# Performance work log

Hardware: AMD Instinct MI355X
Metric: run time of the kernel (lower is better)

## Reference

```python
import jax, jax.numpy as jnp
import numpy as np
from jax import lax

B = 128      # graphs per batch
N = 68       # facial landmarks (num_nodes per graph)
C = 3        # input channels
P = 32       # PATCH_SIZE
K = 16       # NUM_KERNELS
FD = 64      # feature_dim
GH = 128     # gcn_hidden_dim
OUT = 2      # output_dim
EG = 8 * N   # edges per graph
T = B * N    # total nodes


def setup_inputs() -> dict:
    key = jax.random.key(0)
    ks = jax.random.split(key, 8)
    x = jax.random.normal(ks[0], (T, C, P, P), jnp.float32)
    e = jax.random.randint(ks[1], (2, B, EG), 0, N)
    offs = (jnp.arange(B) * N)[None, :, None]
    edge_index = (e + offs).reshape(2, -1)            # within-graph edges, global ids
    batch = jnp.repeat(jnp.arange(B), N)              # node -> graph id
    conv_w = jax.random.normal(ks[2], (N, K, C, 3, 3), jnp.float32) * 0.05
    conv_b = jnp.zeros((N, K), jnp.float32)
    lin1_w = jax.random.normal(ks[3], (N, K * (P // 2) * (P // 2), FD), jnp.float32) * 0.02
    lin1_b = jnp.zeros((N, FD), jnp.float32)
    gcn_w = jax.random.normal(ks[4], (FD, GH), jnp.float32) * 0.1
    gcn_b = jnp.zeros((GH,), jnp.float32)
    mlp_w1 = jax.random.normal(ks[5], (GH, GH // 2), jnp.float32) * 0.1
    mlp_b1 = jnp.zeros((GH // 2,), jnp.float32)
    mlp_w2 = jax.random.normal(ks[6], (GH // 2, OUT), jnp.float32) * 0.1
    mlp_b2 = jnp.zeros((OUT,), jnp.float32)
    return dict(x=x, edge_index=edge_index, batch=batch, conv_w=conv_w, conv_b=conv_b,
                lin1_w=lin1_w, lin1_b=lin1_b, gcn_w=gcn_w, gcn_b=gcn_b,
                mlp_w1=mlp_w1, mlp_b1=mlp_b1, mlp_w2=mlp_w2, mlp_b2=mlp_b2)


def reference(x, edge_index, batch, conv_w, conv_b, lin1_w, lin1_b,
              gcn_w, gcn_b, mlp_w1, mlp_b1, mlp_w2, mlp_b2):
    # --- per-node-type CNN routing (nodes are laid out [graph, local_index]) ---
    xr = x.reshape(B, N, C, P, P)

    def cnn_one(xn, w, b):           # xn: [B,C,P,P]  w: [K,C,3,3]
        y = lax.conv_general_dilated(xn, w, (1, 1), 'SAME',
                                     dimension_numbers=('NCHW', 'OIHW', 'NCHW'))
        return jax.nn.relu(y + b[None, :, None, None])

    a = jax.vmap(cnn_one, in_axes=(1, 0, 0), out_axes=1)(xr, conv_w, conv_b)  # [B,N,K,P,P]
    pooled = lax.reduce_window(a, -jnp.inf, lax.max,
                               (1, 1, 1, 2, 2), (1, 1, 1, 2, 2), 'VALID')     # [B,N,K,P/2,P/2]
    flat = pooled.reshape(B, N, -1)
    feats = jax.nn.relu(jnp.einsum('bnf,nfo->bno', flat, lin1_w) + lin1_b[None])  # [B,N,FD]
    nodes = feats.reshape(T, FD)

    # --- GCNConv: add self-loops, symmetric normalization ---
    loop = jnp.arange(T)
    src = jnp.concatenate([edge_index[0], loop])
    dst = jnp.concatenate([edge_index[1], loop])
    deg = jax.ops.segment_sum(jnp.ones_like(dst, jnp.float32), dst, T)
    dis = jnp.where(deg > 0, 1.0 / jnp.sqrt(deg), 0.0)
    norm = dis[src] * dis[dst]
    xw = nodes @ gcn_w                                   # [T,GH]
    h = jax.ops.segment_sum(norm[:, None] * xw[src], dst, T) + gcn_b
    h = jax.nn.relu(h)

    # --- global mean pool over graphs ---
    cnt = jax.ops.segment_sum(jnp.ones((T,), jnp.float32), batch, B)
    g = jax.ops.segment_sum(h, batch, B) / cnt[:, None]  # [B,GH]

    # --- MLP head ---
    z = jax.nn.relu(g @ mlp_w1 + mlp_b1)
    return z @ mlp_w2 + mlp_b2                           # [B,OUT]
```

## Files before the change

kernel.cpp:

```cpp
#include <hip/hip_runtime.h>
#include <hip/hip_fp16.h>

#define B_   128
#define N_   68
#define C_   3
#define P_   32
#define K_   16
#define FD_  64
#define GH_  128
#define EG_  544
#define T_   8704
#define FLAT_ 4096
#define FCH_ 16

typedef __attribute__((ext_vector_type(8))) _Float16 half8;
typedef __attribute__((ext_vector_type(2))) _Float16 half2v;
typedef __attribute__((ext_vector_type(4))) float   floatx4;
typedef __attribute__((ext_vector_type(4))) unsigned int uint32x4;

#define ROWP 40
#define CHP  1400

__global__ __launch_bounds__(256) void wfrag_prep_kernel(
    const float* __restrict__ conv_w, _Float16* __restrict__ wfrag) {
  const int n = blockIdx.x;
  const int tid = threadIdx.x;
  const float* wp = conv_w + (size_t)n * (K_ * 27);
  _Float16* out = wfrag + (size_t)n * 2048;
  for (int i = tid; i < 2048; i += 256) {
    int sx   = (i >> 10) & 1;
    int type = (i >> 9) & 1;
    int k    = (i >> 5) & 15;
    int slot = i & 31;
    float v = 0.0f;
    if (type == 0) {
      int q = slot >> 3, r = (slot >> 2) & 1, col = slot & 3;
      int cr = q * 2 + r, c = cr / 3, dy = cr - c * 3, dx = col - sx;
      if (dx >= 0 && dx < 3) v = wp[k * 27 + c * 9 + dy * 3 + dx];
    } else {
      int q = slot >> 3, j = slot & 7;
      if (q == 0 && j < 4) {
        int dx = j - sx;
        if (dx >= 0 && dx < 3) v = wp[k * 27 + 24 + dx];
      }
    }
    out[i] = (_Float16)v;
  }
}

__global__ __launch_bounds__(256) void conv_pool_kernel(
    const float* __restrict__ x, const _Float16* __restrict__ wfrag,
    const float* __restrict__ conv_b, _Float16* __restrict__ pooled) {
  const int t = blockIdx.x;
  const int n = t % N_;
  const int tid = threadIdx.x;

  __shared__ _Float16 xsh[3 * CHP];

  const int lane = tid & 63;
  const int lr = lane & 15, q = lane >> 4;
  const int wave = tid >> 6;
  const int ldy = lr >> 3, ldx = lr & 7;

  const float4* xg = (const float4*)(x + (size_t)t * (C_ * P_ * P_));
  float4 xv[3];
  #pragma unroll
  for (int j = 0; j < 3; j++) xv[j] = xg[tid + j * 256];

  const _Float16* wf = wfrag + (size_t)n * 2048 + lr * 32 + q * 8;
  half8 aMain0 = *(const half8*)&wf[0 * 512];
  half8 aCorr0 = *(const half8*)&wf[1 * 512];
  half8 aMain1 = *(const half8*)&wf[2 * 512];
  half8 aCorr1 = *(const half8*)&wf[3 * 512];
  floatx4 cbias = *(const floatx4*)&conv_b[(size_t)n * K_ + q * 4];

  for (int i = tid; i < 396; i += 256) {
    int c = i / 132, j = i - c * 132;
    int off;
    if (j < 34)       off = j;
    else if (j < 68)  off = 33 * ROWP + (j - 34);
    else if (j < 100) off = (j - 68 + 1) * ROWP;
    else              off = (j - 100 + 1) * ROWP + 33;
    xsh[c * CHP + off] = (_Float16)0.0f;
  }
  #pragma unroll
  for (int j = 0; j < 3; j++) {
    int f0 = (tid + j * 256) * 4;
    int c = f0 >> 10, rem = f0 & 1023, y = rem >> 5, xc = rem & 31;
    _Float16* dp = &xsh[c * CHP + (y + 1) * ROWP + xc + 1];
    dp[0] = (_Float16)xv[j].x; dp[1] = (_Float16)xv[j].y;
    dp[2] = (_Float16)xv[j].z; dp[3] = (_Float16)xv[j].w;
  }
  __syncthreads();

  const int crL = q * 2, crH = crL + 1;
  const int cL = crL / 3, dyL = crL - cL * 3;
  const int cH = crH / 3, dyH = crH - cH * 3;
  const _Float16* chL = &xsh[cL * CHP + dyL * ROWP];
  const _Float16* chH = &xsh[cH * CHP + dyH * ROWP];
  const _Float16* chC = &xsh[2 * CHP + 2 * ROWP];

  #pragma unroll
  for (int i = 0; i < 4; i++) {
    const int qq = wave * 4 + i;
    const int py0 = (qq >> 1) * 2, px0 = (qq & 1) * 8;
    const int py = py0 + ldy, px = px0 + ldx;
    const int ebase = py * (2 * ROWP) + px * 2;
    const _Float16* pL = chL + ebase;
    const _Float16* pH = chH + ebase;
    const _Float16* pC = chC + ebase;

    floatx4 mx;
    #pragma unroll
    for (int sy = 0; sy < 2; sy++) {
      unsigned int uL0 = *(const unsigned int*)&pL[sy * ROWP];
      unsigned int uL1 = *(const unsigned int*)&pL[sy * ROWP + 2];
      unsigned int uH0 = *(const unsigned int*)&pH[sy * ROWP];
      unsigned int uH1 = *(const unsigned int*)&pH[sy * ROWP + 2];
      unsigned int uC0 = *(const unsigned int*)&pC[sy * ROWP];
      unsigned int uC1 = *(const unsigned int*)&pC[sy * ROWP + 2];
      half8 bMain = __builtin_bit_cast(half8, (uint32x4){uL0, uL1, uH0, uH1});
      half8 bCorr = __builtin_bit_cast(half8, (uint32x4){uC0, uC1, uC0, uC1});
      floatx4 d0 = __builtin_amdgcn_mfma_f32_16x16x32_f16(aCorr0, bCorr, cbias, 0, 0, 0);
      d0 = __builtin_amdgcn_mfma_f32_16x16x32_f16(aMain0, bMain, d0, 0, 0, 0);
      floatx4 d1 = __builtin_amdgcn_mfma_f32_16x16x32_f16(aCorr1, bCorr, cbias, 0, 0, 0);
      d1 = __builtin_amdgcn_mfma_f32_16x16x32_f16(aMain1, bMain, d1, 0, 0, 0);
      floatx4 m;
      m[0] = fmaxf(d0[0], d1[0]); m[1] = fmaxf(d0[1], d1[1]);
      m[2] = fmaxf(d0[2], d1[2]); m[3] = fmaxf(d0[3], d1[3]);
      if (sy == 0) mx = m;
      else {
        mx[0] = fmaxf(mx[0], m[0]); mx[1] = fmaxf(mx[1], m[1]);
        mx[2] = fmaxf(mx[2], m[2]); mx[3] = fmaxf(mx[3], m[3]);
      }
    }
    _Float16* op = pooled + (size_t)t * FLAT_ + q * 1024 + py * 16 + px;
    op[0]   = (_Float16)fmaxf(mx[0], 0.0f);
    op[256] = (_Float16)fmaxf(mx[1], 0.0f);
    op[512] = (_Float16)fmaxf(mx[2], 0.0f);
    op[768] = (_Float16)fmaxf(mx[3], 0.0f);
  }
}

__global__ __launch_bounds__(256) void lin1_mfma_kernel(
    const _Float16* __restrict__ pooled, const float* __restrict__ lin1_w,
    float* __restrict__ part) {
  const int n   = blockIdx.x >> 4;
  const int fc  = blockIdx.x & 15;
  const int tid = threadIdx.x;
  const int wave = tid >> 6, lane = tid & 63;
  const int q = lane >> 4, lr = lane & 15;

  __shared__ __align__(16) _Float16 As[128 * 72];
  __shared__ __align__(16) _Float16 Bt[64 * 72];

  floatx4 acc[2][4];
  #pragma unroll
  for (int mt = 0; mt < 2; mt++)
    #pragma unroll
    for (int nt = 0; nt < 4; nt++)
      acc[mt][nt] = (floatx4){0.f, 0.f, 0.f, 0.f};

  const int f_base = fc * 256;
  for (int step = 0; step < 4; step++) {
    const int f0 = f_base + step * 64;

    #pragma unroll
    for (int j = 0; j < 4; j++) {
      int idx = tid + j * 256;
      int r = idx >> 3, ch = idx & 7;
      uint4 v = *(const uint4*)&pooled[(size_t)(r * N_ + n) * FLAT_ + f0 + ch * 8];
      *(uint4*)&As[r * 72 + ch * 8] = v;
    }
    const float* wg = &lin1_w[(size_t)n * (FLAT_ * FD_) + (size_t)f0 * FD_];
    #pragma unroll
    for (int it = 0; it < 2; it++) {
      int p = tid + it * 256;
      int o0 = (p & 15) * 4, k0 = (p >> 4) * 2;
      const float* wgk = wg + k0 * 64 + o0;
      float4 va = *(const float4*)wgk;
      float4 vb = *(const float4*)(wgk + 64);
      *(half2v*)&Bt[(o0 + 0) * 72 + k0] = (half2v){(_Float16)va.x, (_Float16)vb.x};
      *(half2v*)&Bt[(o0 + 1) * 72 + k0] = (half2v){(_Float16)va.y, (_Float16)vb.y};
      *(half2v*)&Bt[(o0 + 2) * 72 + k0] = (half2v){(_Float16)va.z, (_Float16)vb.z};
      *(half2v*)&Bt[(o0 + 3) * 72 + k0] = (half2v){(_Float16)va.w, (_Float16)vb.w};
    }
    __syncthreads();

    #pragma unroll
    for (int kh = 0; kh < 2; kh++) {
      half8 af[2], bf[4];
      #pragma unroll
      for (int mt = 0; mt < 2; mt++)
        af[mt] = *(const half8*)&As[(wave * 32 + mt * 16 + lr) * 72 + kh * 32 + q * 8];
      #pragma unroll
      for (int nt = 0; nt < 4; nt++)
        bf[nt] = *(const half8*)&Bt[(nt * 16 + lr) * 72 + kh * 32 + q * 8];
      #pragma unroll
      for (int mt = 0; mt < 2; mt++)
        #pragma unroll
        for (int nt = 0; nt < 4; nt++)
          acc[mt][nt] = __builtin_amdgcn_mfma_f32_16x16x32_f16(
              af[mt], bf[nt], acc[mt][nt], 0, 0, 0);
    }
    __syncthreads();
  }

  float* pb = part + (size_t)fc * T_ * FD_;
  #pragma unroll
  for (int mt = 0; mt < 2; mt++) {
    #pragma unroll
    for (int v = 0; v < 4; v++) {
      int r = wave * 32 + mt * 16 + q * 4 + v;
      size_t base = (size_t)(r * N_ + n) * FD_;
      #pragma unroll
      for (int nt = 0; nt < 4; nt++)
        pb[base + nt * 16 + lr] = acc[mt][nt][v];
    }
  }
}

__global__ __launch_bounds__(256) void feats_kernel(
    const float* __restrict__ part, const float* __restrict__ lin1_b,
    float* __restrict__ feats) {
  int gid = blockIdx.x * 256 + threadIdx.x;
  int t = gid >> 4, f4 = (gid & 15) * 4;
  int n = t % N_;
  float4 s = *(const float4*)&lin1_b[n * FD_ + f4];
  #pragma unroll
  for (int fc = 0; fc < FCH_; fc++) {
    float4 v = *(const float4*)&part[((size_t)fc * T_ + t) * FD_ + f4];
    s.x += v.x; s.y += v.y; s.z += v.z; s.w += v.w;
  }
  s.x = fmaxf(s.x, 0.f); s.y = fmaxf(s.y, 0.f);
  s.z = fmaxf(s.z, 0.f); s.w = fmaxf(s.w, 0.f);
  *(float4*)&feats[(size_t)t * FD_ + f4] = s;
}

__global__ __launch_bounds__(256) void gcn_agg_kernel(
    const float* __restrict__ feats, const int* __restrict__ edge_index,
    float* __restrict__ agg) {
  const int b  = blockIdx.x >> 1;
  const int fh = blockIdx.x & 1;
  const int tid = threadIdx.x;

  __shared__ float fS[N_ * 33], aS[N_ * 33];
  __shared__ int   esrcS[EG_], edstS[EG_];
  __shared__ float nrmS[EG_];
  __shared__ int   degS[N_];
  __shared__ float disS[N_];

  if (tid < N_) degS[tid] = 0;
  const int* srcp = edge_index;
  const int* dstp = edge_index + (B_ * EG_);
  const int e0 = b * EG_, nbase = b * N_;
  for (int e = tid; e < EG_; e += 256) {
    esrcS[e] = srcp[e0 + e] - nbase;
    edstS[e] = dstp[e0 + e] - nbase;
  }
  for (int idx = tid; idx < N_ * 32; idx += 256) {
    int i = idx >> 5, f = idx & 31;
    fS[i * 33 + f] = feats[(size_t)(b * N_ + i) * FD_ + fh * 32 + f];
  }
  __syncthreads();
  for (int e = tid; e < EG_; e += 256) atomicAdd(&degS[edstS[e]], 1);
  __syncthreads();
  if (tid < N_) disS[tid] = rsqrtf((float)(degS[tid] + 1));
  __syncthreads();
  for (int e = tid; e < EG_; e += 256)
    nrmS[e] = disS[esrcS[e]] * disS[edstS[e]];
  for (int idx = tid; idx < N_ * 32; idx += 256) {
    int i = idx >> 5, f = idx & 31;
    float d = disS[i];
    aS[i * 33 + f] = d * d * fS[i * 33 + f];
  }
  __syncthreads();
  for (int idx = tid; idx < EG_ * 32; idx += 256) {
    int e = idx >> 5, f = idx & 31;
    atomicAdd(&aS[edstS[e] * 33 + f], nrmS[e] * fS[esrcS[e] * 33 + f]);
  }
  __syncthreads();
  for (int idx = tid; idx < N_ * 32; idx += 256) {
    int i = idx >> 5, f = idx & 31;
    agg[(size_t)(b * N_ + i) * FD_ + fh * 32 + f] = aS[i * 33 + f];
  }
}

__global__ __launch_bounds__(512) void gcn_head_kernel(
    const float* __restrict__ agg, const float* __restrict__ gcn_w,
    const float* __restrict__ gcn_b, const float* __restrict__ w1,
    const float* __restrict__ b1, const float* __restrict__ w2,
    const float* __restrict__ b2, float* __restrict__ out) {
  const int b = blockIdx.x;
  const int tid = threadIdx.x;

  __shared__ float aS[N_ * 68];
  __shared__ float wS[FD_ * GH_];
  __shared__ float gP[4][GH_];
  __shared__ float z1S[64];

  for (int i4 = tid; i4 < N_ * 16; i4 += 512) {
    int i = i4 >> 4, qf = (i4 & 15) * 4;
    *(float4*)&aS[i * 68 + qf] = *(const float4*)&agg[(size_t)(b * N_ + i) * FD_ + qf];
  }
  #pragma unroll
  for (int j = 0; j < 4; j++)
    ((float4*)wS)[tid + j * 512] = ((const float4*)gcn_w)[tid + j * 512];
  __syncthreads();

  const int j = tid & 127, ig = tid >> 7;
  float wc[64];
  #pragma unroll
  for (int k = 0; k < 64; k++) wc[k] = wS[k * GH_ + j];
  const float bias = gcn_b[j];
  float gsum = 0.f;
  for (int i = ig; i < N_; i += 4) {
    float acc = bias;
    #pragma unroll
    for (int kq = 0; kq < 16; kq++) {
      float4 a = *(const float4*)&aS[i * 68 + kq * 4];
      acc += a.x * wc[kq * 4] + a.y * wc[kq * 4 + 1]
           + a.z * wc[kq * 4 + 2] + a.w * wc[kq * 4 + 3];
    }
    gsum += fmaxf(acc, 0.f);
  }
  gP[ig][j] = gsum;
  __syncthreads();
  if (tid < GH_)
    gP[0][tid] = (gP[0][tid] + gP[1][tid] + gP[2][tid] + gP[3][tid]) * (1.f / 68.f);
  __syncthreads();
  if (tid < 64) {
    float s = b1[tid];
    #pragma unroll 8
    for (int jj = 0; jj < GH_; jj++) s += gP[0][jj] * w1[jj * 64 + tid];
    z1S[tid] = fmaxf(s, 0.f);
  }
  __syncthreads();
  if (tid < 2) {
    float s = b2[tid];
    #pragma unroll 8
    for (int jj = 0; jj < 64; jj++) s += z1S[jj] * w2[jj * 2 + tid];
    out[b * 2 + tid] = s;
  }
}

extern "C" void kernel_launch(void* const* d_in, const int* in_sizes, int n_in,
                              void* d_out, int out_size, void* d_ws, size_t ws_size,
                              hipStream_t stream) {
  const float* x        = (const float*)d_in[0];
  const int*   edge_idx = (const int*)d_in[1];
  const float* conv_w   = (const float*)d_in[3];
  const float* conv_b   = (const float*)d_in[4];
  const float* lin1_w   = (const float*)d_in[5];
  const float* lin1_b   = (const float*)d_in[6];
  const float* gcn_w    = (const float*)d_in[7];
  const float* gcn_b    = (const float*)d_in[8];
  const float* mlp_w1   = (const float*)d_in[9];
  const float* mlp_b1   = (const float*)d_in[10];
  const float* mlp_w2   = (const float*)d_in[11];
  const float* mlp_b2   = (const float*)d_in[12];
  float* outp = (float*)d_out;

  char* wsb = (char*)d_ws;
  _Float16* pooled = (_Float16*)wsb;
  float* part  = (float*)(wsb + (size_t)T_ * FLAT_ * 2);
  float* feats = part + (size_t)FCH_ * T_ * FD_;
  float* agg   = feats + (size_t)T_ * FD_;
  _Float16* wfrag = (_Float16*)(agg + (size_t)T_ * FD_);

  wfrag_prep_kernel<<<N_, 256, 0, stream>>>(conv_w, wfrag);
  conv_pool_kernel<<<T_, 256, 0, stream>>>(x, wfrag, conv_b, pooled);
  lin1_mfma_kernel<<<N_ * FCH_, 256, 0, stream>>>(pooled, lin1_w, part);
  feats_kernel<<<544, 256, 0, stream>>>(part, lin1_b, feats);
  gcn_agg_kernel<<<B_ * 2, 256, 0, stream>>>(feats, edge_idx, agg);
  gcn_head_kernel<<<B_, 512, 0, stream>>>(agg, gcn_w, gcn_b,
                                          mlp_w1, mlp_b1, mlp_w2, mlp_b2, outp);
}
```

Measured before the change: 311.8 us.

## Fuse feats, GCN aggregation and head kernels; process two nodes per conv block

Three tail kernels (partial-sum reduction, GCN aggregation, GCN head) are merged into one per-graph kernel, so the feats and agg intermediates no longer round-trip through global memory and two launches disappear. The lin1 partial outputs are re-laid out as [node][fc][feature] so the fused kernel reads one contiguous chunk per node. The conv_pool kernel now handles two nodes of the same type per block, halving the grid and reusing the weight fragment loads. The tail becomes 128 blocks doing more serial work each, and the conv kernel's shared memory per block doubles, which may lower occupancy.

```diff
diff --git a/kernel.cpp b/kernel.cpp
--- a/kernel.cpp
+++ b/kernel.cpp
@@ -10,6 +10,7 @@
 #define GH_  128
 #define EG_  544
 #define T_   8704
+#define HT_  4352
 #define FLAT_ 4096
 #define FCH_ 16
 
@@ -51,21 +52,24 @@
 __global__ __launch_bounds__(256) void conv_pool_kernel(
     const float* __restrict__ x, const _Float16* __restrict__ wfrag,
     const float* __restrict__ conv_b, _Float16* __restrict__ pooled) {
-  const int t = blockIdx.x;
-  const int n = t % N_;
+  const int t0 = blockIdx.x;
+  const int n = t0 % N_;
   const int tid = threadIdx.x;
 
-  __shared__ _Float16 xsh[3 * CHP];
+  __shared__ _Float16 xsh[2][3 * CHP];
 
   const int lane = tid & 63;
   const int lr = lane & 15, q = lane >> 4;
   const int wave = tid >> 6;
   const int ldy = lr >> 3, ldx = lr & 7;
 
-  const float4* xg = (const float4*)(x + (size_t)t * (C_ * P_ * P_));
-  float4 xv[3];
-  #pragma unroll
-  for (int j = 0; j < 3; j++) xv[j] = xg[tid + j * 256];
+  float4 xv[2][3];
+  #pragma unroll
+  for (int im = 0; im < 2; im++) {
+    const float4* xg = (const float4*)(x + (size_t)(t0 + im * HT_) * (C_ * P_ * P_));
+    #pragma unroll
+    for (int j = 0; j < 3; j++) xv[im][j] = xg[tid + j * 256];
+  }
 
   const _Float16* wf = wfrag + (size_t)n * 2048 + lr * 32 + q * 8;
   half8 aMain0 = *(const half8*)&wf[0 * 512];
@@ -74,71 +78,85 @@
   half8 aCorr1 = *(const half8*)&wf[3 * 512];
   floatx4 cbias = *(const floatx4*)&conv_b[(size_t)n * K_ + q * 4];
 
-  for (int i = tid; i < 396; i += 256) {
-    int c = i / 132, j = i - c * 132;
-    int off;
-    if (j < 34)       off = j;
-    else if (j < 68)  off = 33 * ROWP + (j - 34);
-    else if (j < 100) off = (j - 68 + 1) * ROWP;
-    else              off = (j - 100 + 1) * ROWP + 33;
-    xsh[c * CHP + off] = (_Float16)0.0f;
-  }
-  #pragma unroll
-  for (int j = 0; j < 3; j++) {
-    int f0 = (tid + j * 256) * 4;
-    int c = f0 >> 10, rem = f0 & 1023, y = rem >> 5, xc = rem & 31;
-    _Float16* dp = &xsh[c * CHP + (y + 1) * ROWP + xc + 1];
-    dp[0] = (_Float16)xv[j].x; dp[1] = (_Float16)xv[j].y;
-    dp[2] = (_Float16)xv[j].z; dp[3] = (_Float16)xv[j].w;
+  #pragma unroll
+  for (int im = 0; im < 2; im++) {
+    for (int i = tid; i < 396; i += 256) {
+      int c = i / 132, j = i - c * 132;
+      int off;
+      if (j < 34)       off = j;
+      else if (j < 68)  off = 33 * ROWP + (j - 34);
+      else if (j < 100) off = (j - 68 + 1) * ROWP;
+      else              off = (j - 100 + 1) * ROWP + 33;
+      xsh[im][c * CHP + off] = (_Float16)0.0f;
+    }
+  }
+  #pragma unroll
+  for (int im = 0; im < 2; im++) {
+    #pragma unroll
+    for (int j = 0; j < 3; j++) {
+      int f0 = (tid + j * 256) * 4;
+      int c = f0 >> 10, rem = f0 & 1023, y = rem >> 5, xc = rem & 31;
+      _Float16* dp = &xsh[im][c * CHP + (y + 1) * ROWP + xc + 1];
+      dp[0] = (_Float16)xv[im][j].x; dp[1] = (_Float16)xv[im][j].y;
+      dp[2] = (_Float16)xv[im][j].z; dp[3] = (_Float16)xv[im][j].w;
+    }
   }
   __syncthreads();
 
   const int crL = q * 2, crH = crL + 1;
   const int cL = crL / 3, dyL = crL - cL * 3;
   const int cH = crH / 3, dyH = crH - cH * 3;
-  const _Float16* chL = &xsh[cL * CHP + dyL * ROWP];
-  const _Float16* chH = &xsh[cH * CHP + dyH * ROWP];
-  const _Float16* chC = &xsh[2 * CHP + 2 * ROWP];
-
-  #pragma unroll
-  for (int i = 0; i < 4; i++) {
-    const int qq = wave * 4 + i;
-    const int py0 = (qq >> 1) * 2, px0 = (qq & 1) * 8;
-    const int py = py0 + ldy, px = px0 + ldx;
-    const int ebase = py * (2 * ROWP) + px * 2;
-    const _Float16* pL = chL + ebase;
-    const _Float16* pH = chH + ebase;
-    const _Float16* pC = chC + ebase;
-
-    floatx4 mx;
-    #pragma unroll
-    for (int sy = 0; sy < 2; sy++) {
-      unsigned int uL0 = *(const unsigned int*)&pL[sy * ROWP];
-      unsigned int uL1 = *(const unsigned int*)&pL[sy * ROWP + 2];
-      unsigned int uH0 = *(const unsigned int*)&pH[sy * ROWP];
-      unsigned int uH1 = *(const unsigned int*)&pH[sy * ROWP + 2];
-      unsigned int uC0 = *(const unsigned int*)&pC[sy * ROWP];
-      unsigned int uC1 = *(const unsigned int*)&pC[sy * ROWP + 2];
-      half8 bMain = __builtin_bit_cast(half8, (uint32x4){uL0, uL1, uH0, uH1});
-      half8 bCorr = __builtin_bit_cast(half8, (uint32x4){uC0, uC1, uC0, uC1});
-      floatx4 d0 = __builtin_amdgcn_mfma_f32_16x16x32_f16(aCorr0, bCorr, cbias, 0, 0, 0);
-      d0 = __builtin_amdgcn_mfma_f32_16x16x32_f16(aMain0, bMain, d0, 0, 0, 0);
-      floatx4 d1 = __builtin_amdgcn_mfma_f32_16x16x32_f16(aCorr1, bCorr, cbias, 0, 0, 0);
-      d1 = __builtin_amdgcn_mfma_f32_16x16x32_f16(aMain1, bMain, d1, 0, 0, 0);
-      floatx4 m;
-      m[0] = fmaxf(d0[0], d1[0]); m[1] = fmaxf(d0[1], d1[1]);
-      m[2] = fmaxf(d0[2], d1[2]); m[3] = fmaxf(d0[3], d1[3]);
-      if (sy == 0) mx = m;
-      else {
-        mx[0] = fmaxf(mx[0], m[0]); mx[1] = fmaxf(mx[1], m[1]);
-        mx[2] = fmaxf(mx[2], m[2]); mx[3] = fmaxf(mx[3], m[3]);
+  const int offL = cL * CHP + dyL * ROWP;
+  const int offH = cH * CHP + dyH * ROWP;
+  const int offC = 2 * CHP + 2 * ROWP;
+
+  #pragma unroll
+  for (int im = 0; im < 2; im++) {
+    const _Float16* chL = &xsh[im][offL];
+    const _Float16* chH = &xsh[im][offH];
+    const _Float16* chC = &xsh[im][offC];
+    const size_t tcur = (size_t)(t0 + im * HT_);
+
+    #pragma unroll
+    for (int i = 0; i < 4; i++) {
+      const int qq = wave * 4 + i;
+      const int py0 = (qq >> 1) * 2, px0 = (qq & 1) * 8;
+      const int py = py0 + ldy, px = px0 + ldx;
+      const int ebase = py * (2 * ROWP) + px * 2;
+      const _Float16* pL = chL + ebase;
+      const _Float16* pH = chH + ebase;
+      const _Float16* pC = chC + ebase;
+
+      floatx4 mx;
+      #pragma unroll
+      for (int sy = 0; sy < 2; sy++) {
+        unsigned int uL0 = *(const unsigned int*)&pL[sy * ROWP];
+        unsigned int uL1 = *(const unsigned int*)&pL[sy * ROWP + 2];
+        unsigned int uH0 = *(const unsigned int*)&pH[sy * ROWP];
+        unsigned int uH1 = *(const unsigned int*)&pH[sy * ROWP + 2];
+        unsigned int uC0 = *(const unsigned int*)&pC[sy * ROWP];
+        unsigned int uC1 = *(const unsigned int*)&pC[sy * ROWP + 2];
+        half8 bMain = __builtin_bit_cast(half8, (uint32x4){uL0, uL1, uH0, uH1});
+        half8 bCorr = __builtin_bit_cast(half8, (uint32x4){uC0, uC1, uC0, uC1});
+        floatx4 d0 = __builtin_amdgcn_mfma_f32_16x16x32_f16(aCorr0, bCorr, cbias, 0, 0, 0);
+        d0 = __builtin_amdgcn_mfma_f32_16x16x32_f16(aMain0, bMain, d0, 0, 0, 0);
+        floatx4 d1 = __builtin_amdgcn_mfma_f32_16x16x32_f16(aCorr1, bCorr, cbias, 0, 0, 0);
+        d1 = __builtin_amdgcn_mfma_f32_16x16x32_f16(aMain1, bMain, d1, 0, 0, 0);
+        floatx4 m;
+        m[0] = fmaxf(d0[0], d1[0]); m[1] = fmaxf(d0[1], d1[1]);
+        m[2] = fmaxf(d0[2], d1[2]); m[3] = fmaxf(d0[3], d1[3]);
+        if (sy == 0) mx = m;
+        else {
+          mx[0] = fmaxf(mx[0], m[0]); mx[1] = fmaxf(mx[1], m[1]);
+          mx[2] = fmaxf(mx[2], m[2]); mx[3] = fmaxf(mx[3], m[3]);
+        }
       }
-    }
-    _Float16* op = pooled + (size_t)t * FLAT_ + q * 1024 + py * 16 + px;
-    op[0]   = (_Float16)fmaxf(mx[0], 0.0f);
-    op[256] = (_Float16)fmaxf(mx[1], 0.0f);
-    op[512] = (_Float16)fmaxf(mx[2], 0.0f);
-    op[768] = (_Float16)fmaxf(mx[3], 0.0f);
+      _Float16* op = pooled + tcur * FLAT_ + q * 1024 + py * 16 + px;
+      op[0]   = (_Float16)fmaxf(mx[0], 0.0f);
+      op[256] = (_Float16)fmaxf(mx[1], 0.0f);
+      op[512] = (_Float16)fmaxf(mx[2], 0.0f);
+      op[768] = (_Float16)fmaxf(mx[3], 0.0f);
+    }
   }
 }
 
@@ -206,106 +224,73 @@
     __syncthreads();
   }
 
-  float* pb = part + (size_t)fc * T_ * FD_;
   #pragma unroll
   for (int mt = 0; mt < 2; mt++) {
     #pragma unroll
     for (int v = 0; v < 4; v++) {
       int r = wave * 32 + mt * 16 + q * 4 + v;
-      size_t base = (size_t)(r * N_ + n) * FD_;
+      size_t base = ((size_t)(r * N_ + n) * FCH_ + fc) * FD_;
       #pragma unroll
       for (int nt = 0; nt < 4; nt++)
-        pb[base + nt * 16 + lr] = acc[mt][nt][v];
-    }
-  }
-}
-
-__global__ __launch_bounds__(256) void feats_kernel(
+        part[base + nt * 16 + lr] = acc[mt][nt][v];
+    }
+  }
+}
+
+__global__ __launch_bounds__(512) void gcn_tail_kernel(
     const float* __restrict__ part, const float* __restrict__ lin1_b,
-    float* __restrict__ feats) {
-  int gid = blockIdx.x * 256 + threadIdx.x;
-  int t = gid >> 4, f4 = (gid & 15) * 4;
-  int n = t % N_;
-  float4 s = *(const float4*)&lin1_b[n * FD_ + f4];
-  #pragma unroll
-  for (int fc = 0; fc < FCH_; fc++) {
-    float4 v = *(const float4*)&part[((size_t)fc * T_ + t) * FD_ + f4];
-    s.x += v.x; s.y += v.y; s.z += v.z; s.w += v.w;
-  }
-  s.x = fmaxf(s.x, 0.f); s.y = fmaxf(s.y, 0.f);
-  s.z = fmaxf(s.z, 0.f); s.w = fmaxf(s.w, 0.f);
-  *(float4*)&feats[(size_t)t * FD_ + f4] = s;
-}
-
-__global__ __launch_bounds__(256) void gcn_agg_kernel(
-    const float* __restrict__ feats, const int* __restrict__ edge_index,
-    float* __restrict__ agg) {
-  const int b  = blockIdx.x >> 1;
-  const int fh = blockIdx.x & 1;
-  const int tid = threadIdx.x;
-
-  __shared__ float fS[N_ * 33], aS[N_ * 33];
-  __shared__ int   esrcS[EG_], edstS[EG_];
-  __shared__ float nrmS[EG_];
-  __shared__ int   degS[N_];
-  __shared__ float disS[N_];
-
-  if (tid < N_) degS[tid] = 0;
-  const int* srcp = edge_index;
-  const int* dstp = edge_index + (B_ * EG_);
-  const int e0 = b * EG_, nbase = b * N_;
-  for (int e = tid; e < EG_; e += 256) {
-    esrcS[e] = srcp[e0 + e] - nbase;
-    edstS[e] = dstp[e0 + e] - nbase;
-  }
-  for (int idx = tid; idx < N_ * 32; idx += 256) {
-    int i = idx >> 5, f = idx & 31;
-    fS[i * 33 + f] = feats[(size_t)(b * N_ + i) * FD_ + fh * 32 + f];
-  }
-  __syncthreads();
-  for (int e = tid; e < EG_; e += 256) atomicAdd(&degS[edstS[e]], 1);
-  __syncthreads();
-  if (tid < N_) disS[tid] = rsqrtf((float)(degS[tid] + 1));
-  __syncthreads();
-  for (int e = tid; e < EG_; e += 256)
-    nrmS[e] = disS[esrcS[e]] * disS[edstS[e]];
-  for (int idx = tid; idx < N_ * 32; idx += 256) {
-    int i = idx >> 5, f = idx & 31;
-    float d = disS[i];
-    aS[i * 33 + f] = d * d * fS[i * 33 + f];
-  }
-  __syncthreads();
-  for (int idx = tid; idx < EG_ * 32; idx += 256) {
-    int e = idx >> 5, f = idx & 31;
-    atomicAdd(&aS[edstS[e] * 33 + f], nrmS[e] * fS[esrcS[e] * 33 + f]);
-  }
-  __syncthreads();
-  for (int idx = tid; idx < N_ * 32; idx += 256) {
-    int i = idx >> 5, f = idx & 31;
-    agg[(size_t)(b * N_ + i) * FD_ + fh * 32 + f] = aS[i * 33 + f];
-  }
-}
-
-__global__ __launch_bounds__(512) void gcn_head_kernel(
-    const float* __restrict__ agg, const float* __restrict__ gcn_w,
+    const int* __restrict__ edge_index, const float* __restrict__ gcn_w,
     const float* __restrict__ gcn_b, const float* __restrict__ w1,
     const float* __restrict__ b1, const float* __restrict__ w2,
     const float* __restrict__ b2, float* __restrict__ out) {
   const int b = blockIdx.x;
   const int tid = threadIdx.x;
 
-  __shared__ float aS[N_ * 68];
+  __shared__ float fS[N_ * 64], aS[N_ * 64];
+  __shared__ int   esrcS[EG_], edstS[EG_];
+  __shared__ float nrmS[EG_];
+  __shared__ int   degS[N_];
+  __shared__ float disS[N_];
   __shared__ float wS[FD_ * GH_];
   __shared__ float gP[4][GH_];
   __shared__ float z1S[64];
 
-  for (int i4 = tid; i4 < N_ * 16; i4 += 512) {
-    int i = i4 >> 4, qf = (i4 & 15) * 4;
-    *(float4*)&aS[i * 68 + qf] = *(const float4*)&agg[(size_t)(b * N_ + i) * FD_ + qf];
+  if (tid < N_) degS[tid] = 0;
+  const int* srcp = edge_index;
+  const int* dstp = edge_index + (B_ * EG_);
+  const int e0 = b * EG_, nbase = b * N_;
+  for (int e = tid; e < EG_; e += 512) {
+    esrcS[e] = srcp[e0 + e] - nbase;
+    edstS[e] = dstp[e0 + e] - nbase;
   }
   #pragma unroll
   for (int j = 0; j < 4; j++)
     ((float4*)wS)[tid + j * 512] = ((const float4*)gcn_w)[tid + j * 512];
+  for (int idx = tid; idx < N_ * 64; idx += 512) {
+    int i = idx >> 6, f = idx & 63;
+    const float* pp = &part[(size_t)((b * N_ + i) * FCH_) * FD_ + f];
+    float s = lin1_b[i * FD_ + f];
+    #pragma unroll
+    for (int fc = 0; fc < FCH_; fc++) s += pp[fc * FD_];
+    fS[idx] = fmaxf(s, 0.f);
+  }
+  __syncthreads();
+  for (int e = tid; e < EG_; e += 512) atomicAdd(&degS[edstS[e]], 1);
+  __syncthreads();
+  if (tid < N_) disS[tid] = rsqrtf((float)(degS[tid] + 1));
+  __syncthreads();
+  for (int e = tid; e < EG_; e += 512)
+    nrmS[e] = disS[esrcS[e]] * disS[edstS[e]];
+  for (int idx = tid; idx < N_ * 64; idx += 512) {
+    int i = idx >> 6;
+    float d = disS[i];
+    aS[idx] = d * d * fS[idx];
+  }
+  __syncthreads();
+  for (int idx = tid; idx < EG_ * 64; idx += 512) {
+    int e = idx >> 6, f = idx & 63;
+    atomicAdd(&aS[edstS[e] * 64 + f], nrmS[e] * fS[esrcS[e] * 64 + f]);
+  }
   __syncthreads();
 
   const int j = tid & 127, ig = tid >> 7;
@@ -318,7 +303,7 @@
     float acc = bias;
     #pragma unroll
     for (int kq = 0; kq < 16; kq++) {
-      float4 a = *(const float4*)&aS[i * 68 + kq * 4];
+      float4 a = *(const float4*)&aS[i * 64 + kq * 4];
       acc += a.x * wc[kq * 4] + a.y * wc[kq * 4 + 1]
            + a.z * wc[kq * 4 + 2] + a.w * wc[kq * 4 + 3];
     }
@@ -364,15 +349,11 @@
   char* wsb = (char*)d_ws;
   _Float16* pooled = (_Float16*)wsb;
   float* part  = (float*)(wsb + (size_t)T_ * FLAT_ * 2);
-  float* feats = part + (size_t)FCH_ * T_ * FD_;
-  float* agg   = feats + (size_t)T_ * FD_;
-  _Float16* wfrag = (_Float16*)(agg + (size_t)T_ * FD_);
+  _Float16* wfrag = (_Float16*)(part + (size_t)T_ * FCH_ * FD_);
 
   wfrag_prep_kernel<<<N_, 256, 0, stream>>>(conv_w, wfrag);
-  conv_pool_kernel<<<T_, 256, 0, stream>>>(x, wfrag, conv_b, pooled);
+  conv_pool_kernel<<<HT_, 256, 0, stream>>>(x, wfrag, conv_b, pooled);
   lin1_mfma_kernel<<<N_ * FCH_, 256, 0, stream>>>(pooled, lin1_w, part);
-  feats_kernel<<<544, 256, 0, stream>>>(part, lin1_b, feats);
-  gcn_agg_kernel<<<B_ * 2, 256, 0, stream>>>(feats, edge_idx, agg);
-  gcn_head_kernel<<<B_, 512, 0, stream>>>(agg, gcn_w, gcn_b,
+  gcn_tail_kernel<<<B_, 512, 0, stream>>>(part, lin1_b, edge_idx, gcn_w, gcn_b,
                                           mlp_w1, mlp_b1, mlp_w2, mlp_b2, outp);
 }
```

New measurement: 327.9 us. 1.05x slower.

## Process two nodes per conv block and reorder lin1 partial-sum layout

Applied to the files above, without the earlier changes.

The conv+pool kernel now handles two node images per block, t0 and t0+4352. 4352 is a multiple of 68, so both share the same node type and weight fragments, and the grid is halved. This amortises the weight-fragment loads and launch overhead and raises bytes in flight per block, at the cost of twice the shared memory and more registers. Separately, the lin1 partial buffer is re-laid out as [node][chunk][feature], so the reduction in feats_kernel reads contiguous memory. In exchange, the MFMA kernel's stores become more strided.

```diff
diff --git a/kernel.cpp b/kernel.cpp
--- a/kernel.cpp
+++ b/kernel.cpp
@@ -10,6 +10,7 @@
 #define GH_  128
 #define EG_  544
 #define T_   8704
+#define HT_  4352
 #define FLAT_ 4096
 #define FCH_ 16
 
@@ -51,21 +52,24 @@
 __global__ __launch_bounds__(256) void conv_pool_kernel(
     const float* __restrict__ x, const _Float16* __restrict__ wfrag,
     const float* __restrict__ conv_b, _Float16* __restrict__ pooled) {
-  const int t = blockIdx.x;
-  const int n = t % N_;
-  const int tid = threadIdx.x;
-
-  __shared__ _Float16 xsh[3 * CHP];
+  const int t0 = blockIdx.x;
+  const int n = t0 % N_;
+  const int tid = threadIdx.x;
+
+  __shared__ _Float16 xsh[2][3 * CHP];
 
   const int lane = tid & 63;
   const int lr = lane & 15, q = lane >> 4;
   const int wave = tid >> 6;
   const int ldy = lr >> 3, ldx = lr & 7;
 
-  const float4* xg = (const float4*)(x + (size_t)t * (C_ * P_ * P_));
-  float4 xv[3];
-  #pragma unroll
-  for (int j = 0; j < 3; j++) xv[j] = xg[tid + j * 256];
+  float4 xv[2][3];
+  #pragma unroll
+  for (int im = 0; im < 2; im++) {
+    const float4* xg = (const float4*)(x + (size_t)(t0 + im * HT_) * (C_ * P_ * P_));
+    #pragma unroll
+    for (int j = 0; j < 3; j++) xv[im][j] = xg[tid + j * 256];
+  }
 
   const _Float16* wf = wfrag + (size_t)n * 2048 + lr * 32 + q * 8;
   half8 aMain0 = *(const half8*)&wf[0 * 512];
@@ -74,71 +78,85 @@
   half8 aCorr1 = *(const half8*)&wf[3 * 512];
   floatx4 cbias = *(const floatx4*)&conv_b[(size_t)n * K_ + q * 4];
 
-  for (int i = tid; i < 396; i += 256) {
-    int c = i / 132, j = i - c * 132;
-    int off;
-    if (j < 34)       off = j;
-    else if (j < 68)  off = 33 * ROWP + (j - 34);
-    else if (j < 100) off = (j - 68 + 1) * ROWP;
-    else              off = (j - 100 + 1) * ROWP + 33;
-    xsh[c * CHP + off] = (_Float16)0.0f;
-  }
-  #pragma unroll
-  for (int j = 0; j < 3; j++) {
-    int f0 = (tid + j * 256) * 4;
-    int c = f0 >> 10, rem = f0 & 1023, y = rem >> 5, xc = rem & 31;
-    _Float16* dp = &xsh[c * CHP + (y + 1) * ROWP + xc + 1];
-    dp[0] = (_Float16)xv[j].x; dp[1] = (_Float16)xv[j].y;
-    dp[2] = (_Float16)xv[j].z; dp[3] = (_Float16)xv[j].w;
+  #pragma unroll
+  for (int im = 0; im < 2; im++) {
+    for (int i = tid; i < 396; i += 256) {
+      int c = i / 132, j = i - c * 132;
+      int off;
+      if (j < 34)       off = j;
+      else if (j < 68)  off = 33 * ROWP + (j - 34);
+      else if (j < 100) off = (j - 68 + 1) * ROWP;
+      else              off = (j - 100 + 1) * ROWP + 33;
+      xsh[im][c * CHP + off] = (_Float16)0.0f;
+    }
+  }
+  #pragma unroll
+  for (int im = 0; im < 2; im++) {
+    #pragma unroll
+    for (int j = 0; j < 3; j++) {
+      int f0 = (tid + j * 256) * 4;
+      int c = f0 >> 10, rem = f0 & 1023, y = rem >> 5, xc = rem & 31;
+      _Float16* dp = &xsh[im][c * CHP + (y + 1) * ROWP + xc + 1];
+      dp[0] = (_Float16)xv[im][j].x; dp[1] = (_Float16)xv[im][j].y;
+      dp[2] = (_Float16)xv[im][j].z; dp[3] = (_Float16)xv[im][j].w;
+    }
   }
   __syncthreads();
 
   const int crL = q * 2, crH = crL + 1;
   const int cL = crL / 3, dyL = crL - cL * 3;
   const int cH = crH / 3, dyH = crH - cH * 3;
-  const _Float16* chL = &xsh[cL * CHP + dyL * ROWP];
-  const _Float16* chH = &xsh[cH * CHP + dyH * ROWP];
-  const _Float16* chC = &xsh[2 * CHP + 2 * ROWP];
-
-  #pragma unroll
-  for (int i = 0; i < 4; i++) {
-    const int qq = wave * 4 + i;
-    const int py0 = (qq >> 1) * 2, px0 = (qq & 1) * 8;
-    const int py = py0 + ldy, px = px0 + ldx;
-    const int ebase = py * (2 * ROWP) + px * 2;
-    const _Float16* pL = chL + ebase;
-    const _Float16* pH = chH + ebase;
-    const _Float16* pC = chC + ebase;
-
-    floatx4 mx;
-    #pragma unroll
-    for (int sy = 0; sy < 2; sy++) {
-      unsigned int uL0 = *(const unsigned int*)&pL[sy * ROWP];
-      unsigned int uL1 = *(const unsigned int*)&pL[sy * ROWP + 2];
-      unsigned int uH0 = *(const unsigned int*)&pH[sy * ROWP];
-      unsigned int uH1 = *(const unsigned int*)&pH[sy * ROWP + 2];
-      unsigned int uC0 = *(const unsigned int*)&pC[sy * ROWP];
-      unsigned int uC1 = *(const unsigned int*)&pC[sy * ROWP + 2];
-      half8 bMain = __builtin_bit_cast(half8, (uint32x4){uL0, uL1, uH0, uH1});
-      half8 bCorr = __builtin_bit_cast(half8, (uint32x4){uC0, uC1, uC0, uC1});
-      floatx4 d0 = __builtin_amdgcn_mfma_f32_16x16x32_f16(aCorr0, bCorr, cbias, 0, 0, 0);
-      d0 = __builtin_amdgcn_mfma_f32_16x16x32_f16(aMain0, bMain, d0, 0, 0, 0);
-      floatx4 d1 = __builtin_amdgcn_mfma_f32_16x16x32_f16(aCorr1, bCorr, cbias, 0, 0, 0);
-      d1 = __builtin_amdgcn_mfma_f32_16x16x32_f16(aMain1, bMain, d1, 0, 0, 0);
-      floatx4 m;
-      m[0] = fmaxf(d0[0], d1[0]); m[1] = fmaxf(d0[1], d1[1]);
-      m[2] = fmaxf(d0[2], d1[2]); m[3] = fmaxf(d0[3], d1[3]);
-      if (sy == 0) mx = m;
-      else {
-        mx[0] = fmaxf(mx[0], m[0]); mx[1] = fmaxf(mx[1], m[1]);
-        mx[2] = fmaxf(mx[2], m[2]); mx[3] = fmaxf(mx[3], m[3]);
+  const int offL = cL * CHP + dyL * ROWP;
+  const int offH = cH * CHP + dyH * ROWP;
+  const int offC = 2 * CHP + 2 * ROWP;
+
+  #pragma unroll
+  for (int im = 0; im < 2; im++) {
+    const _Float16* chL = &xsh[im][offL];
+    const _Float16* chH = &xsh[im][offH];
+    const _Float16* chC = &xsh[im][offC];
+    const size_t tcur = (size_t)(t0 + im * HT_);
+
+    #pragma unroll
+    for (int i = 0; i < 4; i++) {
+      const int qq = wave * 4 + i;
+      const int py0 = (qq >> 1) * 2, px0 = (qq & 1) * 8;
+      const int py = py0 + ldy, px = px0 + ldx;
+      const int ebase = py * (2 * ROWP) + px * 2;
+      const _Float16* pL = chL + ebase;
+      const _Float16* pH = chH + ebase;
+      const _Float16* pC = chC + ebase;
+
+      floatx4 mx;
+      #pragma unroll
+      for (int sy = 0; sy < 2; sy++) {
+        unsigned int uL0 = *(const unsigned int*)&pL[sy * ROWP];
+        unsigned int uL1 = *(const unsigned int*)&pL[sy * ROWP + 2];
+        unsigned int uH0 = *(const unsigned int*)&pH[sy * ROWP];
+        unsigned int uH1 = *(const unsigned int*)&pH[sy * ROWP + 2];
+        unsigned int uC0 = *(const unsigned int*)&pC[sy * ROWP];
+        unsigned int uC1 = *(const unsigned int*)&pC[sy * ROWP + 2];
+        half8 bMain = __builtin_bit_cast(half8, (uint32x4){uL0, uL1, uH0, uH1});
+        half8 bCorr = __builtin_bit_cast(half8, (uint32x4){uC0, uC1, uC0, uC1});
+        floatx4 d0 = __builtin_amdgcn_mfma_f32_16x16x32_f16(aCorr0, bCorr, cbias, 0, 0, 0);
+        d0 = __builtin_amdgcn_mfma_f32_16x16x32_f16(aMain0, bMain, d0, 0, 0, 0);
+        floatx4 d1 = __builtin_amdgcn_mfma_f32_16x16x32_f16(aCorr1, bCorr, cbias, 0, 0, 0);
+        d1 = __builtin_amdgcn_mfma_f32_16x16x32_f16(aMain1, bMain, d1, 0, 0, 0);
+        floatx4 m;
+        m[0] = fmaxf(d0[0], d1[0]); m[1] = fmaxf(d0[1], d1[1]);
+        m[2] = fmaxf(d0[2], d1[2]); m[3] = fmaxf(d0[3], d1[3]);
+        if (sy == 0) mx = m;
+        else {
+          mx[0] = fmaxf(mx[0], m[0]); mx[1] = fmaxf(mx[1], m[1]);
+          mx[2] = fmaxf(mx[2], m[2]); mx[3] = fmaxf(mx[3], m[3]);
+        }
       }
-    }
-    _Float16* op = pooled + (size_t)t * FLAT_ + q * 1024 + py * 16 + px;
-    op[0]   = (_Float16)fmaxf(mx[0], 0.0f);
-    op[256] = (_Float16)fmaxf(mx[1], 0.0f);
-    op[512] = (_Float16)fmaxf(mx[2], 0.0f);
-    op[768] = (_Float16)fmaxf(mx[3], 0.0f);
+      _Float16* op = pooled + tcur * FLAT_ + q * 1024 + py * 16 + px;
+      op[0]   = (_Float16)fmaxf(mx[0], 0.0f);
+      op[256] = (_Float16)fmaxf(mx[1], 0.0f);
+      op[512] = (_Float16)fmaxf(mx[2], 0.0f);
+      op[768] = (_Float16)fmaxf(mx[3], 0.0f);
+    }
   }
 }
 
@@ -206,16 +224,15 @@
     __syncthreads();
   }
 
-  float* pb = part + (size_t)fc * T_ * FD_;
   #pragma unroll
   for (int mt = 0; mt < 2; mt++) {
     #pragma unroll
     for (int v = 0; v < 4; v++) {
       int r = wave * 32 + mt * 16 + q * 4 + v;
-      size_t base = (size_t)(r * N_ + n) * FD_;
+      size_t base = ((size_t)(r * N_ + n) * FCH_ + fc) * FD_;
       #pragma unroll
       for (int nt = 0; nt < 4; nt++)
-        pb[base + nt * 16 + lr] = acc[mt][nt][v];
+        part[base + nt * 16 + lr] = acc[mt][nt][v];
     }
   }
 }
@@ -226,10 +243,11 @@
   int gid = blockIdx.x * 256 + threadIdx.x;
   int t = gid >> 4, f4 = (gid & 15) * 4;
   int n = t % N_;
+  const float* pp = &part[(size_t)t * FCH_ * FD_ + f4];
   float4 s = *(const float4*)&lin1_b[n * FD_ + f4];
   #pragma unroll
   for (int fc = 0; fc < FCH_; fc++) {
-    float4 v = *(const float4*)&part[((size_t)fc * T_ + t) * FD_ + f4];
+    float4 v = *(const float4*)&pp[fc * FD_];
     s.x += v.x; s.y += v.y; s.z += v.z; s.w += v.w;
   }
   s.x = fmaxf(s.x, 0.f); s.y = fmaxf(s.y, 0.f);
@@ -364,12 +382,12 @@
   char* wsb = (char*)d_ws;
   _Float16* pooled = (_Float16*)wsb;
   float* part  = (float*)(wsb + (size_t)T_ * FLAT_ * 2);
-  float* feats = part + (size_t)FCH_ * T_ * FD_;
+  float* feats = part + (size_t)T_ * FCH_ * FD_;
   float* agg   = feats + (size_t)T_ * FD_;
   _Float16* wfrag = (_Float16*)(agg + (size_t)T_ * FD_);
 
   wfrag_prep_kernel<<<N_, 256, 0, stream>>>(conv_w, wfrag);
-  conv_pool_kernel<<<T_, 256, 0, stream>>>(x, wfrag, conv_b, pooled);
+  conv_pool_kernel<<<HT_, 256, 0, stream>>>(x, wfrag, conv_b, pooled);
   lin1_mfma_kernel<<<N_ * FCH_, 256, 0, stream>>>(pooled, lin1_w, part);
   feats_kernel<<<544, 256, 0, stream>>>(part, lin1_b, feats);
   gcn_agg_kernel<<<B_ * 2, 256, 0, stream>>>(feats, edge_idx, agg);
```

New measurement: 317.3 us. About the same (+1.8%).

## Prefetch lin1 tiles into registers, store fp16 partials, fuse feats reduction into aggregation

Applied to the files above, without the earlier changes.

The lin1 MFMA kernel now loads the next step's pooled and weight tiles into registers while the current tile is computed, with one barrier per step instead of two. Partial sums are written in fp16 in a node-major layout rather than fp32. The separate feats reduction kernel is removed, and the partial-sum reduction, bias and ReLU now happen inside the GCN aggregation kernel. This cuts a launch and intermediate memory traffic, at the cost of extra register pressure and lower precision in the partial sums.

```diff
diff --git a/kernel.cpp b/kernel.cpp
--- a/kernel.cpp
+++ b/kernel.cpp
@@ -14,6 +14,7 @@
 #define FCH_ 16
 
 typedef __attribute__((ext_vector_type(8))) _Float16 half8;
+typedef __attribute__((ext_vector_type(4))) _Float16 half4v;
 typedef __attribute__((ext_vector_type(2))) _Float16 half2v;
 typedef __attribute__((ext_vector_type(4))) float   floatx4;
 typedef __attribute__((ext_vector_type(4))) unsigned int uint32x4;
@@ -144,7 +145,7 @@
 
 __global__ __launch_bounds__(256) void lin1_mfma_kernel(
     const _Float16* __restrict__ pooled, const float* __restrict__ lin1_w,
-    float* __restrict__ part) {
+    _Float16* __restrict__ part) {
   const int n   = blockIdx.x >> 4;
   const int fc  = blockIdx.x & 15;
   const int tid = threadIdx.x;
@@ -162,29 +163,44 @@
       acc[mt][nt] = (floatx4){0.f, 0.f, 0.f, 0.f};
 
   const int f_base = fc * 256;
+  const float* wg = &lin1_w[(size_t)n * (FLAT_ * FD_)];
+
+  const int Ab = tid >> 3, Ach8 = (tid & 7) * 8;
+  const int o0 = (tid & 15) * 4;
+  const int k0a = (tid >> 4) * 2;
+  const int k0b = k0a + 32;
+
+  uint4 aR[4];
+  float4 vaR[2], vbR[2];
+
+#define L1_LOADA(step_) { const int f0 = f_base + (step_) * 64;               \
+    _Pragma("unroll")                                                         \
+    for (int j = 0; j < 4; j++)                                               \
+      aR[j] = *(const uint4*)&pooled[(size_t)((Ab + j * 32) * N_ + n) * FLAT_ \
+                                     + f0 + Ach8]; }
+#define L1_LOADB(step_) { const int f0 = f_base + (step_) * 64;               \
+    const float* wgk0 = wg + (size_t)f0 * FD_ + k0a * 64 + o0;                \
+    vaR[0] = *(const float4*)wgk0; vbR[0] = *(const float4*)(wgk0 + 64);      \
+    const float* wgk1 = wg + (size_t)f0 * FD_ + k0b * 64 + o0;                \
+    vaR[1] = *(const float4*)wgk1; vbR[1] = *(const float4*)(wgk1 + 64); }
+
+  L1_LOADA(0); L1_LOADB(0);
+
   for (int step = 0; step < 4; step++) {
-    const int f0 = f_base + step * 64;
-
-    #pragma unroll
-    for (int j = 0; j < 4; j++) {
-      int idx = tid + j * 256;
-      int r = idx >> 3, ch = idx & 7;
-      uint4 v = *(const uint4*)&pooled[(size_t)(r * N_ + n) * FLAT_ + f0 + ch * 8];
-      *(uint4*)&As[r * 72 + ch * 8] = v;
-    }
-    const float* wg = &lin1_w[(size_t)n * (FLAT_ * FD_) + (size_t)f0 * FD_];
+    if (step) __syncthreads();
+    #pragma unroll
+    for (int j = 0; j < 4; j++)
+      *(uint4*)&As[(Ab + j * 32) * 72 + Ach8] = aR[j];
     #pragma unroll
     for (int it = 0; it < 2; it++) {
-      int p = tid + it * 256;
-      int o0 = (p & 15) * 4, k0 = (p >> 4) * 2;
-      const float* wgk = wg + k0 * 64 + o0;
-      float4 va = *(const float4*)wgk;
-      float4 vb = *(const float4*)(wgk + 64);
-      *(half2v*)&Bt[(o0 + 0) * 72 + k0] = (half2v){(_Float16)va.x, (_Float16)vb.x};
-      *(half2v*)&Bt[(o0 + 1) * 72 + k0] = (half2v){(_Float16)va.y, (_Float16)vb.y};
-      *(half2v*)&Bt[(o0 + 2) * 72 + k0] = (half2v){(_Float16)va.z, (_Float16)vb.z};
-      *(half2v*)&Bt[(o0 + 3) * 72 + k0] = (half2v){(_Float16)va.w, (_Float16)vb.w};
-    }
+      const int kk = it ? k0b : k0a;
+      const float4 va = vaR[it], vb = vbR[it];
+      *(half2v*)&Bt[(o0 + 0) * 72 + kk] = (half2v){(_Float16)va.x, (_Float16)vb.x};
+      *(half2v*)&Bt[(o0 + 1) * 72 + kk] = (half2v){(_Float16)va.y, (_Float16)vb.y};
+      *(half2v*)&Bt[(o0 + 2) * 72 + kk] = (half2v){(_Float16)va.z, (_Float16)vb.z};
+      *(half2v*)&Bt[(o0 + 3) * 72 + kk] = (half2v){(_Float16)va.w, (_Float16)vb.w};
+    }
+    if (step < 3) { L1_LOADA(step + 1); L1_LOADB(step + 1); }
     __syncthreads();
 
     #pragma unroll
@@ -203,43 +219,26 @@
           acc[mt][nt] = __builtin_amdgcn_mfma_f32_16x16x32_f16(
               af[mt], bf[nt], acc[mt][nt], 0, 0, 0);
     }
-    __syncthreads();
-  }
-
-  float* pb = part + (size_t)fc * T_ * FD_;
+  }
+#undef L1_LOADA
+#undef L1_LOADB
+
   #pragma unroll
   for (int mt = 0; mt < 2; mt++) {
     #pragma unroll
     for (int v = 0; v < 4; v++) {
       int r = wave * 32 + mt * 16 + q * 4 + v;
-      size_t base = (size_t)(r * N_ + n) * FD_;
+      size_t base = ((size_t)(r * N_ + n) * FCH_ + fc) * FD_;
       #pragma unroll
       for (int nt = 0; nt < 4; nt++)
-        pb[base + nt * 16 + lr] = acc[mt][nt][v];
-    }
-  }
-}
-
-__global__ __launch_bounds__(256) void feats_kernel(
-    const float* __restrict__ part, const float* __restrict__ lin1_b,
-    float* __restrict__ feats) {
-  int gid = blockIdx.x * 256 + threadIdx.x;
-  int t = gid >> 4, f4 = (gid & 15) * 4;
-  int n = t % N_;
-  float4 s = *(const float4*)&lin1_b[n * FD_ + f4];
-  #pragma unroll
-  for (int fc = 0; fc < FCH_; fc++) {
-    float4 v = *(const float4*)&part[((size_t)fc * T_ + t) * FD_ + f4];
-    s.x += v.x; s.y += v.y; s.z += v.z; s.w += v.w;
-  }
-  s.x = fmaxf(s.x, 0.f); s.y = fmaxf(s.y, 0.f);
-  s.z = fmaxf(s.z, 0.f); s.w = fmaxf(s.w, 0.f);
-  *(float4*)&feats[(size_t)t * FD_ + f4] = s;
-}
-
-__global__ __launch_bounds__(256) void gcn_agg_kernel(
-    const float* __restrict__ feats, const int* __restrict__ edge_index,
-    float* __restrict__ agg) {
+        part[base + nt * 16 + lr] = (_Float16)acc[mt][nt][v];
+    }
+  }
+}
+
+__global__ __launch_bounds__(256) void featagg_kernel(
+    const _Float16* __restrict__ part, const float* __restrict__ lin1_b,
+    const int* __restrict__ edge_index, float* __restrict__ agg) {
   const int b  = blockIdx.x >> 1;
   const int fh = blockIdx.x & 1;
   const int tid = threadIdx.x;
@@ -258,9 +257,19 @@
     esrcS[e] = srcp[e0 + e] - nbase;
     edstS[e] = dstp[e0 + e] - nbase;
   }
-  for (int idx = tid; idx < N_ * 32; idx += 256) {
-    int i = idx >> 5, f = idx & 31;
-    fS[i * 33 + f] = feats[(size_t)(b * N_ + i) * FD_ + fh * 32 + f];
+  for (int u = tid; u < N_ * 8; u += 256) {
+    int i = u >> 3, f4 = (u & 7) * 4;
+    const _Float16* pp = &part[((size_t)(b * N_ + i) * FCH_) * FD_ + fh * 32 + f4];
+    float4 s = *(const float4*)&lin1_b[i * FD_ + fh * 32 + f4];
+    #pragma unroll
+    for (int fc = 0; fc < FCH_; fc++) {
+      half4v v = *(const half4v*)&pp[fc * FD_];
+      s.x += (float)v[0]; s.y += (float)v[1];
+      s.z += (float)v[2]; s.w += (float)v[3];
+    }
+    float* fp = &fS[i * 33 + f4];
+    fp[0] = fmaxf(s.x, 0.f); fp[1] = fmaxf(s.y, 0.f);
+    fp[2] = fmaxf(s.z, 0.f); fp[3] = fmaxf(s.w, 0.f);
   }
   __syncthreads();
   for (int e = tid; e < EG_; e += 256) atomicAdd(&degS[edstS[e]], 1);
@@ -363,16 +372,14 @@
 
   char* wsb = (char*)d_ws;
   _Float16* pooled = (_Float16*)wsb;
-  float* part  = (float*)(wsb + (size_t)T_ * FLAT_ * 2);
-  float* feats = part + (size_t)FCH_ * T_ * FD_;
-  float* agg   = feats + (size_t)T_ * FD_;
-  _Float16* wfrag = (_Float16*)(agg + (size_t)T_ * FD_);
+  _Float16* part   = pooled + (size_t)T_ * FLAT_;
+  float* agg       = (float*)(part + (size_t)T_ * FCH_ * FD_);
+  _Float16* wfrag  = (_Float16*)(agg + (size_t)T_ * FD_);
 
   wfrag_prep_kernel<<<N_, 256, 0, stream>>>(conv_w, wfrag);
   conv_pool_kernel<<<T_, 256, 0, stream>>>(x, wfrag, conv_b, pooled);
   lin1_mfma_kernel<<<N_ * FCH_, 256, 0, stream>>>(pooled, lin1_w, part);
-  feats_kernel<<<544, 256, 0, stream>>>(part, lin1_b, feats);
-  gcn_agg_kernel<<<B_ * 2, 256, 0, stream>>>(feats, edge_idx, agg);
+  featagg_kernel<<<B_ * 2, 256, 0, stream>>>(part, lin1_b, edge_idx, agg);
   gcn_head_kernel<<<B_, 512, 0, stream>>>(agg, gcn_w, gcn_b,
                                           mlp_w1, mlp_b1, mlp_w2, mlp_b2, outp);
 }
```

Measured after the change: 316.2 us. Within noise of the previous version (+1.4%).
